# Kernel tuning notes

Measured on AMD Instinct MI355X. Metric: run time of the kernel, lower is better.

The kernel has to match this reference:

```python
import jax, jax.numpy as jnp
import numpy as np

# Model dims (init_kwargs): in_channels=hid_channels=128, freq_bins=64, num_heads=8
B, CIN, HID, FREQ, T, H = 4, 128, 128, 64, 512, 8
EPS = 1e-5  # LayerNormalization4D eps


def _conv_act_norm(y, w, b, alpha, gamma, beta):
    """1x1 Conv2d + PReLU + LayerNormalization4D(C,F) on [B, C_in, T, F].
    w: [C_out, C_in], b: [C_out], alpha: scalar PReLU slope,
    gamma/beta: [1, C_out, 1, F]; normalize over (channel, freq) dims."""
    y = jnp.einsum('bctf,oc->botf', y, w) + b[None, :, None, None]
    y = jnp.where(y >= 0, y, alpha * y)  # PReLU (single shared slope)
    mu = jnp.mean(y, axis=(1, 3), keepdims=True)
    var = jnp.mean(jnp.square(y - mu), axis=(1, 3), keepdims=True)
    return (y - mu) / jnp.sqrt(var + EPS) * gamma + beta


def setup_inputs() -> dict:
    key = jax.random.key(0)
    ks = jax.random.split(key, 6)
    s = 0.02
    return {
        'x': jax.random.normal(ks[0], (B, CIN, FREQ, T), jnp.float32),
        'qkv_w': jax.random.normal(ks[1], (3 * HID, CIN), jnp.float32) * s,
        'qkv_b': jnp.zeros((3 * HID,), jnp.float32),
        'qkv_alpha': jnp.float32(0.25),
        'qkv_gamma': jnp.ones((1, 3 * HID, 1, FREQ), jnp.float32),
        'qkv_beta': jnp.zeros((1, 3 * HID, 1, FREQ), jnp.float32),
        'proj_w': jax.random.normal(ks[2], (CIN, CIN), jnp.float32) * s,
        'proj_b': jnp.zeros((CIN,), jnp.float32),
        'proj_alpha': jnp.float32(0.25),
        'proj_gamma': jnp.ones((1, CIN, 1, FREQ), jnp.float32),
        'proj_beta': jnp.zeros((1, CIN, 1, FREQ), jnp.float32),
    }


def reference(x, qkv_w, qkv_b, qkv_alpha, qkv_gamma, qkv_beta,
              proj_w, proj_b, proj_alpha, proj_gamma, proj_beta):
    # x: [B, C, F, T] -> [B, C, T, F]
    xt = jnp.swapaxes(x, -2, -1)
    qkv = _conv_act_norm(xt, qkv_w, qkv_b, qkv_alpha, qkv_gamma, qkv_beta)  # [B, 3*HID, T, F]
    # [B, T, 3*HID, F] -> heads split over flattened (channel, freq) axis
    qkv = jnp.swapaxes(qkv, 1, 2).reshape(B, T, H, -1)
    qkv = jnp.swapaxes(qkv, 1, 2)  # [B, H, T, 3*hd]
    hd = qkv.shape[-1] // 3
    q = qkv[..., :hd]
    k = qkv[..., hd:2 * hd]
    v = qkv[..., 2 * hd:]
    scores = jnp.einsum('bhqd,bhkd->bhqk', q, k) * (hd ** -0.5)
    causal = jnp.triu(jnp.ones((T, T), bool), 1)
    scores = jnp.where(causal[None, None], -jnp.inf, scores)
    attn = jax.nn.softmax(scores, axis=-1)
    ctx = jnp.einsum('bhqk,bhkd->bhqd', attn, v)  # [B, H, T, hd]
    # mimic torch: reshape(B*H, T, hd).transpose(1,2).reshape(B, HID, T, FREQ)
    c = jnp.swapaxes(ctx.reshape(B * H, T, hd), 1, 2).reshape(B, HID, T, FREQ)
    out = _conv_act_norm(c, proj_w, proj_b, proj_alpha, proj_gamma, proj_beta)
    return jnp.swapaxes(out, 2, 3)  # [B, C, F, T]
```

## Files before the change

kernel.cpp:

```cpp
#include <hip/hip_runtime.h>
#include <hip/hip_bf16.h>

#define T_    512
#define CIN_  128
#define OC1   384
#define NH    8
#define HD    1024

using sh8 = __attribute__((ext_vector_type(8))) short;
using fx4 = __attribute__((ext_vector_type(4))) float;

__device__ __forceinline__ short bf16r(float x) {
  union { float f; unsigned u; } v; v.f = x;
  unsigned u = v.u;
  u += 0x7fffu + ((u >> 16) & 1u);
  return (short)(u >> 16);
}
__device__ __forceinline__ float b2f(short s) {
  union { float f; unsigned u; } v; v.u = ((unsigned)(unsigned short)s) << 16;
  return v.f;
}
__device__ __forceinline__ fx4 mfma_bf16(sh8 a, sh8 b, fx4 c) {
  return __builtin_amdgcn_mfma_f32_16x16x32_bf16(a, b, c, 0, 0, 0);
}

__global__ void k_prep(const float* __restrict__ qw, const float* __restrict__ pw,
                       short* __restrict__ qwb, short* __restrict__ pwb) {
  const int i = blockIdx.x * 256 + threadIdx.x;
  if (i < OC1 * CIN_) qwb[i] = bf16r(qw[i]);
  if (i < 128 * 128)  pwb[i] = bf16r(pw[i]);
}

__global__ __launch_bounds__(512) void kA_qkv(
    const float* __restrict__ x, const short* __restrict__ wb,
    const float* __restrict__ bias, const float* __restrict__ alphap,
    short* __restrict__ Qt, short* __restrict__ Kt, short* __restrict__ Vt,
    float* __restrict__ Pstat)
{
  const int bid = blockIdx.x;
  const int b = bid >> 8, f = (bid >> 2) & 63, tt = bid & 3;
  const int tid = threadIdx.x, lane = tid & 63, w = tid >> 6;

  __shared__ short Xs[128 * 128];
  __shared__ float psum[8 * 8 * 16 * 2];

  {
    const int c = tid & 127, tg = tid >> 7;
    const float* xp = x + ((size_t)(b * 128 + c) * 64 + f) * 512 + tt * 128 + tg * 32;
    #pragma unroll
    for (int i = 0; i < 8; ++i) {
      const float4 fv = *(const float4*)(xp + i * 4);
      #pragma unroll
      for (int j = 0; j < 4; ++j) {
        const int t = tg * 32 + i * 4 + j;
        *((short*)((char*)Xs + t * 256 + ((2 * c) ^ ((t & 7) << 4)))) = bf16r((&fv.x)[j]);
      }
    }
  }
  __syncthreads();

  const float alpha = alphap[0];
  fx4 acc[3][8];
  #pragma unroll
  for (int mi = 0; mi < 3; ++mi)
    #pragma unroll
    for (int ni = 0; ni < 8; ++ni) acc[mi][ni] = fx4{0.f, 0.f, 0.f, 0.f};

  #pragma unroll
  for (int ks = 0; ks < 4; ++ks) {
    sh8 a[3];
    #pragma unroll
    for (int mi = 0; mi < 3; ++mi) {
      const int o = w * 48 + mi * 16 + (lane & 15);
      a[mi] = *(const sh8*)(wb + o * 128 + ks * 32 + (lane >> 4) * 8);
    }
    #pragma unroll
    for (int ni = 0; ni < 8; ++ni) {
      const int t = ni * 16 + (lane & 15);
      const int kb = ks * 64 + (lane >> 4) * 16;
      const sh8 bf = *(const sh8*)((const char*)Xs + t * 256 + (kb ^ ((t & 7) << 4)));
      #pragma unroll
      for (int mi = 0; mi < 3; ++mi)
        acc[mi][ni] = mfma_bf16(a[mi], bf, acc[mi][ni]);
    }
  }

  float s0[8], s1[8];
  #pragma unroll
  for (int ni = 0; ni < 8; ++ni) { s0[ni] = 0.f; s1[ni] = 0.f; }
  #pragma unroll
  for (int mi = 0; mi < 3; ++mi)
    #pragma unroll
    for (int r = 0; r < 4; ++r) {
      const int o = w * 48 + mi * 16 + (lane >> 4) * 4 + r;
      const float bo = bias[o];
      #pragma unroll
      for (int ni = 0; ni < 8; ++ni) {
        float v = acc[mi][ni][r] + bo;
        v = (v >= 0.f) ? v : alpha * v;
        acc[mi][ni][r] = v;
        s0[ni] += v; s1[ni] += v * v;
      }
    }
  #pragma unroll
  for (int ni = 0; ni < 8; ++ni) {
    float a0 = s0[ni], a1 = s1[ni];
    a0 += __shfl_down(a0, 32); a1 += __shfl_down(a1, 32);
    a0 += __shfl_down(a0, 16); a1 += __shfl_down(a1, 16);
    if (lane < 16) {
      psum[((w * 8 + ni) * 16 + lane) * 2 + 0] = a0;
      psum[((w * 8 + ni) * 16 + lane) * 2 + 1] = a1;
    }
  }
  __syncthreads();
  if (tid < 256) {
    const int col = tid & 127, s = tid >> 7;
    const int ni = col >> 4, l = col & 15;
    float a0 = 0.f;
    #pragma unroll
    for (int ww = 0; ww < 8; ++ww) a0 += psum[((ww * 8 + ni) * 16 + l) * 2 + s];
    Pstat[(size_t)s * 131072 + (size_t)b * 32768 + (size_t)f * 512 + tt * 128 + col] = a0;
  }

  const int bh = b * 8 + w;
  #pragma unroll
  for (int mi = 0; mi < 3; ++mi) {
    short* dst = (mi == 0) ? Qt : (mi == 1) ? Kt : Vt;
    #pragma unroll
    for (int r = 0; r < 4; ++r) {
      const int cl = (lane >> 4) * 4 + r;
      const int d = cl * 64 + f;
      short* rowp = dst + ((size_t)bh * 1024 + d) * 512 + tt * 128;
      #pragma unroll
      for (int ni = 0; ni < 8; ++ni)
        rowp[ni * 16 + (lane & 15)] = bf16r(acc[mi][ni][r]);
    }
  }
}

__global__ __launch_bounds__(256) void kB_norm(
    const short* __restrict__ Qt, const short* __restrict__ Kt, short* __restrict__ Vt,
    const float* __restrict__ Pstat,
    const float* __restrict__ gamma, const float* __restrict__ beta,
    short* __restrict__ Q, short* __restrict__ K)
{
  const int bid = blockIdx.x;
  const int bh = bid >> 4, tc = bid & 15;
  const int b = bh >> 3, h = bh & 7;
  const int tid = threadIdx.x, lane = tid & 63, w = tid >> 6;
  const int t0 = tc * 32;

  __shared__ short Lt[32 * 512];
  __shared__ float stats[32][2];

  #pragma unroll
  for (int k = 0; k < 8; ++k) {
    const int tl = w * 8 + k;
    const int t = t0 + tl;
    float p0 = Pstat[(size_t)b * 32768 + (size_t)lane * 512 + t];
    float p1 = Pstat[131072 + (size_t)b * 32768 + (size_t)lane * 512 + t];
    #pragma unroll
    for (int off = 32; off > 0; off >>= 1) { p0 += __shfl_down(p0, off); p1 += __shfl_down(p1, off); }
    if (lane == 0) {
      const float mu = p0 * (1.f / 24576.f);
      const float var = p1 * (1.f / 24576.f) - mu * mu;
      stats[tl][0] = mu;
      stats[tl][1] = rsqrtf(var + 1e-5f);
    }
  }
  __syncthreads();

  for (int sect = 0; sect < 2; ++sect) {
    const short* src = sect ? Kt : Qt;
    short* dstq = sect ? K : Q;
    for (int dh = 0; dh < 2; ++dh) {
      __syncthreads();
      #pragma unroll
      for (int rr = 0; rr < 2; ++rr) {
        const int dl = tid + rr * 256;
        const int d = dh * 512 + dl;
        const int gi = (h * 48 + sect * 16 + (d >> 6)) * 64 + (d & 63);
        const float g = gamma[gi], be = beta[gi];
        const short* srow = src + ((size_t)bh * 1024 + d) * 512 + t0;
        #pragma unroll
        for (int i = 0; i < 4; ++i) {
          const sh8 vv = *(const sh8*)(srow + i * 8);
          #pragma unroll
          for (int j = 0; j < 8; ++j) {
            const int tl = i * 8 + j;
            const float z = (b2f(vv[j]) - stats[tl][0]) * stats[tl][1] * g + be;
            *((short*)((char*)Lt + tl * 1024 + ((2 * dl) ^ ((tl & 7) << 4)))) = bf16r(z);
          }
        }
      }
      __syncthreads();
      const int tl = tid >> 3;
      short* orow = dstq + ((size_t)bh * 512 + (t0 + tl)) * 1024 + dh * 512;
      #pragma unroll
      for (int it = 0; it < 8; ++it) {
        const int c16 = (tid & 7) + it * 8;
        const sh8 vv = *(const sh8*)((const char*)Lt + tl * 1024 + ((c16 * 16) ^ ((tl & 7) << 4)));
        *(sh8*)(orow + c16 * 8) = vv;
      }
    }
  }

  #pragma unroll
  for (int rr = 0; rr < 4; ++rr) {
    const int d = tid + rr * 256;
    const int gi = (h * 48 + 32 + (d >> 6)) * 64 + (d & 63);
    const float g = gamma[gi], be = beta[gi];
    short* vrow = Vt + ((size_t)bh * 1024 + d) * 512 + t0;
    #pragma unroll
    for (int i = 0; i < 4; ++i) {
      sh8 vv = *(const sh8*)(vrow + i * 8);
      #pragma unroll
      for (int j = 0; j < 8; ++j) {
        const int tl = i * 8 + j;
        vv[j] = bf16r((b2f(vv[j]) - stats[tl][0]) * stats[tl][1] * g + be);
      }
      *(sh8*)(vrow + i * 8) = vv;
    }
  }
}

__global__ __launch_bounds__(256) void k_qk(
    const short* __restrict__ Q, const short* __restrict__ K, float* __restrict__ S)
{
  const int bid = blockIdx.x;
  const int bh = bid / 10;
  const int j = bid - bh * 10;
  const int qi = (j >= 6) ? 3 : (j >= 3) ? 2 : (j >= 1) ? 1 : 0;
  const int ki = j - qi * (qi + 1) / 2;
  const int tid = threadIdx.x, lane = tid & 63, w = tid >> 6;
  const int wm = w >> 1, wn = w & 1;

  __shared__ short Qs[128 * 64];
  __shared__ short Ks[128 * 64];

  const short* Qg = Q + ((size_t)bh * 512 + qi * 128) * 1024;
  const short* Kg = K + ((size_t)bh * 512 + ki * 128) * 1024;

  fx4 acc[4][4];
  #pragma unroll
  for (int mi = 0; mi < 4; ++mi)
    #pragma unroll
    for (int ni = 0; ni < 4; ++ni) acc[mi][ni] = fx4{0.f, 0.f, 0.f, 0.f};

  for (int ks = 0; ks < 16; ++ks) {
    __syncthreads();
    const int row = tid & 127, kh = tid >> 7;
    #pragma unroll
    for (int i = 0; i < 4; ++i) {
      const int kl = kh * 32 + i * 8;
      const sh8 qv = *(const sh8*)(Qg + (size_t)row * 1024 + ks * 64 + kl);
      const sh8 kv = *(const sh8*)(Kg + (size_t)row * 1024 + ks * 64 + kl);
      *(sh8*)((char*)Qs + row * 128 + ((2 * kl) ^ ((row & 7) << 4))) = qv;
      *(sh8*)((char*)Ks + row * 128 + ((2 * kl) ^ ((row & 7) << 4))) = kv;
    }
    __syncthreads();
    #pragma unroll
    for (int ksub = 0; ksub < 2; ++ksub) {
      sh8 a[4], bf[4];
      #pragma unroll
      for (int mi = 0; mi < 4; ++mi) {
        const int r2 = wm * 64 + mi * 16 + (lane & 15);
        a[mi] = *(const sh8*)((const char*)Qs + r2 * 128 + ((ksub * 64 + (lane >> 4) * 16) ^ ((r2 & 7) << 4)));
      }
      #pragma unroll
      for (int ni = 0; ni < 4; ++ni) {
        const int r2 = wn * 64 + ni * 16 + (lane & 15);
        bf[ni] = *(const sh8*)((const char*)Ks + r2 * 128 + ((ksub * 64 + (lane >> 4) * 16) ^ ((r2 & 7) << 4)));
      }
      #pragma unroll
      for (int mi = 0; mi < 4; ++mi)
        #pragma unroll
        for (int ni = 0; ni < 4; ++ni)
          acc[mi][ni] = mfma_bf16(a[mi], bf[ni], acc[mi][ni]);
    }
  }

  float* Sg = S + (size_t)bh * 262144;
  const int q0 = qi * 128 + wm * 64, k0 = ki * 128 + wn * 64;
  #pragma unroll
  for (int mi = 0; mi < 4; ++mi)
    #pragma unroll
    for (int ni = 0; ni < 4; ++ni) {
      const int q = q0 + mi * 16 + (lane >> 4) * 4;
      const int kc = k0 + ni * 16 + (lane & 15);
      #pragma unroll
      for (int r = 0; r < 4; ++r)
        Sg[(size_t)(q + r) * 512 + kc] = acc[mi][ni][r] * 0.03125f;
    }
}

__global__ __launch_bounds__(256) void k_softmax(const float* __restrict__ S,
                                                 short* __restrict__ Pb)
{
  const int row = blockIdx.x * 4 + (threadIdx.x >> 6);
  const int lane = threadIdx.x & 63;
  const int bh = row >> 9, q = row & 511;
  const float* Sr = S + (size_t)bh * 262144 + (size_t)q * 512;
  short* Pr = Pb + (size_t)bh * 262144 + (size_t)q * 512;
  const int n = q + 1;
  float v[8]; float mx = -1e30f;
  #pragma unroll
  for (int i = 0; i < 8; ++i) {
    const int k = lane + i * 64;
    v[i] = (k < n) ? Sr[k] : -1e30f;
    mx = fmaxf(mx, v[i]);
  }
  #pragma unroll
  for (int off = 32; off > 0; off >>= 1) mx = fmaxf(mx, __shfl_xor(mx, off));
  float sum = 0.f;
  #pragma unroll
  for (int i = 0; i < 8; ++i) {
    const float e = (v[i] > -1e29f) ? __expf(v[i] - mx) : 0.f;
    v[i] = e; sum += e;
  }
  #pragma unroll
  for (int off = 32; off > 0; off >>= 1) sum += __shfl_xor(sum, off);
  const float inv = 1.f / sum;
  #pragma unroll
  for (int i = 0; i < 8; ++i) Pr[lane + i * 64] = bf16r(v[i] * inv);
}

__global__ __launch_bounds__(256) void k_pv(
    const short* __restrict__ Pb, const short* __restrict__ Vt, short* __restrict__ Cs)
{
  const int bid = blockIdx.x;
  const int bh = bid >> 5;
  const int qi = (bid >> 3) & 3, dt = bid & 7;
  const int tid = threadIdx.x, lane = tid & 63, w = tid >> 6;
  const int wm = w >> 1, wn = w & 1;

  __shared__ short Ps[128 * 64];
  __shared__ short Vs[128 * 64];
  __shared__ short ctile[128 * 128];

  const short* Pg = Pb + ((size_t)bh * 512 + qi * 128) * 512;
  const short* Vg = Vt + ((size_t)bh * 1024 + dt * 128) * 512;

  fx4 acc[4][4];
  #pragma unroll
  for (int mi = 0; mi < 4; ++mi)
    #pragma unroll
    for (int ni = 0; ni < 4; ++ni) acc[mi][ni] = fx4{0.f, 0.f, 0.f, 0.f};

  const int nks = (qi + 1) * 2;
  for (int ks = 0; ks < nks; ++ks) {
    __syncthreads();
    const int row = tid & 127, kh = tid >> 7;
    #pragma unroll
    for (int i = 0; i < 4; ++i) {
      const int kl = kh * 32 + i * 8;
      const sh8 pv = *(const sh8*)(Pg + (size_t)row * 512 + ks * 64 + kl);
      const sh8 vv = *(const sh8*)(Vg + (size_t)row * 512 + ks * 64 + kl);
      *(sh8*)((char*)Ps + row * 128 + ((2 * kl) ^ ((row & 7) << 4))) = pv;
      *(sh8*)((char*)Vs + row * 128 + ((2 * kl) ^ ((row & 7) << 4))) = vv;
    }
    __syncthreads();
    #pragma unroll
    for (int ksub = 0; ksub < 2; ++ksub) {
      sh8 a[4], bf[4];
      #pragma unroll
      for (int mi = 0; mi < 4; ++mi) {
        const int r2 = wm * 64 + mi * 16 + (lane & 15);
        a[mi] = *(const sh8*)((const char*)Ps + r2 * 128 + ((ksub * 64 + (lane >> 4) * 16) ^ ((r2 & 7) << 4)));
      }
      #pragma unroll
      for (int ni = 0; ni < 4; ++ni) {
        const int r2 = wn * 64 + ni * 16 + (lane & 15);
        bf[ni] = *(const sh8*)((const char*)Vs + r2 * 128 + ((ksub * 64 + (lane >> 4) * 16) ^ ((r2 & 7) << 4)));
      }
      #pragma unroll
      for (int mi = 0; mi < 4; ++mi)
        #pragma unroll
        for (int ni = 0; ni < 4; ++ni)
          acc[mi][ni] = mfma_bf16(a[mi], bf[ni], acc[mi][ni]);
    }
  }

  #pragma unroll
  for (int mi = 0; mi < 4; ++mi)
    #pragma unroll
    for (int ni = 0; ni < 4; ++ni) {
      const int ql = wm * 64 + mi * 16 + (lane >> 4) * 4;
      const int dl = wn * 64 + ni * 16 + (lane & 15);
      const int swz = (dl & 7) << 4;
      #pragma unroll
      for (int r = 0; r < 4; ++r)
        ctile[(dl * 256 + ((2 * (ql + r)) ^ swz)) >> 1] = bf16r(acc[mi][ni][r]);
    }
  __syncthreads();

  const int b = bh >> 3, h = bh & 7;
  const int cl_loc = tid >> 7, fq = (tid >> 1) & 63, tg_loc = tid & 1;
  const int C = h * 16 + dt * 2 + cl_loc;
  const int t2 = fq * 8 + qi * 2 + tg_loc;
  const int dl = cl_loc * 64 + fq;
  const int swz = (dl & 7) << 4;
  short* dst = Cs + (((size_t)b * 128 + C) * 512 + t2) * 64;
  #pragma unroll
  for (int jj = 0; jj < 8; ++jj) {
    const sh8 vv = *(const sh8*)((const char*)ctile + dl * 256 + ((tg_loc * 128 + jj * 16) ^ swz));
    *(sh8*)(dst + jj * 8) = vv;
  }
}

__global__ __launch_bounds__(512) void k_proj(
    const short* __restrict__ Cs, const short* __restrict__ wb,
    const float* __restrict__ bias, const float* __restrict__ alphap,
    const float* __restrict__ gamma, const float* __restrict__ beta,
    float* __restrict__ Otmp)
{
  const int bid = blockIdx.x;
  const int b = bid >> 9, t2 = bid & 511;
  const int tid = threadIdx.x, lane = tid & 63, w = tid >> 6;

  __shared__ short Xs[64 * 128];
  __shared__ float red[18];

  {
    const int C = tid & 127, fq = tid >> 7;
    const short* srow = Cs + (((size_t)b * 128 + C) * 512 + t2) * 64;
    #pragma unroll
    for (int i = 0; i < 2; ++i) {
      const int fc = fq * 2 + i;
      const sh8 vv = *(const sh8*)(srow + fc * 8);
      #pragma unroll
      for (int jj = 0; jj < 8; ++jj) {
        const int f2 = fc * 8 + jj;
        *((short*)((char*)Xs + f2 * 256 + ((2 * C) ^ ((f2 & 7) << 4)))) = vv[jj];
      }
    }
  }
  __syncthreads();

  const float alpha = alphap[0];
  fx4 acc[4];
  #pragma unroll
  for (int ni = 0; ni < 4; ++ni) acc[ni] = fx4{0.f, 0.f, 0.f, 0.f};

  #pragma unroll
  for (int ks = 0; ks < 4; ++ks) {
    const int o = w * 16 + (lane & 15);
    const sh8 a = *(const sh8*)(wb + o * 128 + ks * 32 + (lane >> 4) * 8);
    #pragma unroll
    for (int ni = 0; ni < 4; ++ni) {
      const int f2 = ni * 16 + (lane & 15);
      const sh8 bf = *(const sh8*)((const char*)Xs + f2 * 256 + ((ks * 64 + (lane >> 4) * 16) ^ ((f2 & 7) << 4)));
      acc[ni] = mfma_bf16(a, bf, acc[ni]);
    }
  }

  float s0 = 0.f, s1 = 0.f;
  const int ob = w * 16 + (lane >> 4) * 4;
  #pragma unroll
  for (int ni = 0; ni < 4; ++ni)
    #pragma unroll
    for (int r = 0; r < 4; ++r) {
      float v = acc[ni][r] + bias[ob + r];
      v = (v >= 0.f) ? v : alpha * v;
      acc[ni][r] = v;
      s0 += v; s1 += v * v;
    }
  #pragma unroll
  for (int off = 32; off > 0; off >>= 1) { s0 += __shfl_down(s0, off); s1 += __shfl_down(s1, off); }
  if (lane == 0) { red[w * 2] = s0; red[w * 2 + 1] = s1; }
  __syncthreads();
  if (tid == 0) {
    float a0 = 0.f, a1 = 0.f;
    for (int i2 = 0; i2 < 8; ++i2) { a0 += red[2 * i2]; a1 += red[2 * i2 + 1]; }
    const float mu = a0 / 8192.f;
    const float var = a1 / 8192.f - mu * mu;
    red[16] = mu; red[17] = rsqrtf(var + 1e-5f);
  }
  __syncthreads();
  const float mu = red[16], rstd = red[17];

  #pragma unroll
  for (int ni = 0; ni < 4; ++ni) {
    const int f2 = ni * 16 + (lane & 15);
    #pragma unroll
    for (int r = 0; r < 4; ++r) {
      const int o = ob + r;
      const float zz = (acc[ni][r] - mu) * rstd * gamma[o * 64 + f2] + beta[o * 64 + f2];
      Otmp[(((size_t)b * 128 + o) * 512 + t2) * 64 + f2] = zz;
    }
  }
}

__global__ __launch_bounds__(256) void k_trans(const float* __restrict__ Otmp,
                                               float* __restrict__ out)
{
  const int bid = blockIdx.x;
  const int bo = bid >> 3, tt8 = bid & 7;
  const int t20 = tt8 * 64;
  const int tid = threadIdx.x;
  __shared__ float Ltr[64][65];
  {
    const int f2c = tid & 15, t2l0 = tid >> 4;
    #pragma unroll
    for (int it = 0; it < 4; ++it) {
      const int t2l = t2l0 + it * 16;
      const float4 fv = *(const float4*)(Otmp + ((size_t)bo * 512 + t20 + t2l) * 64 + f2c * 4);
      Ltr[f2c * 4 + 0][t2l] = fv.x;
      Ltr[f2c * 4 + 1][t2l] = fv.y;
      Ltr[f2c * 4 + 2][t2l] = fv.z;
      Ltr[f2c * 4 + 3][t2l] = fv.w;
    }
  }
  __syncthreads();
  {
    const int t2c = tid & 15, f2l0 = tid >> 4;
    #pragma unroll
    for (int it = 0; it < 4; ++it) {
      const int f2 = f2l0 + it * 16;
      float4 fv;
      fv.x = Ltr[f2][t2c * 4 + 0]; fv.y = Ltr[f2][t2c * 4 + 1];
      fv.z = Ltr[f2][t2c * 4 + 2]; fv.w = Ltr[f2][t2c * 4 + 3];
      *(float4*)(out + ((size_t)bo * 64 + f2) * 512 + t20 + t2c * 4) = fv;
    }
  }
}

extern "C" void kernel_launch(void* const* d_in, const int* in_sizes, int n_in,
                              void* d_out, int out_size, void* d_ws, size_t ws_size,
                              hipStream_t stream) {
  (void)in_sizes; (void)n_in; (void)out_size;
  const float* x          = (const float*)d_in[0];
  const float* qkv_w      = (const float*)d_in[1];
  const float* qkv_b      = (const float*)d_in[2];
  const float* qkv_alpha  = (const float*)d_in[3];
  const float* qkv_gamma  = (const float*)d_in[4];
  const float* qkv_beta   = (const float*)d_in[5];
  const float* proj_w     = (const float*)d_in[6];
  const float* proj_b     = (const float*)d_in[7];
  const float* proj_alpha = (const float*)d_in[8];
  const float* proj_gamma = (const float*)d_in[9];
  const float* proj_beta  = (const float*)d_in[10];
  float* out = (float*)d_out;

  char* ws = (char*)d_ws;
  short* Qt  = (short*)(ws + 0);
  short* Kt  = (short*)(ws + 33554432);
  short* Vt  = (short*)(ws + 67108864);
  short* Q   = (short*)(ws + 100663296);
  short* K   = (short*)(ws + 134217728);
  short* qwb = (short*)(ws + 167772160);
  short* pwb = (short*)(ws + 167870464);
  float* S    = (float*)(ws + 0);
  short* Pb   = (short*)(ws + 33554432);
  short* Cs   = (short*)(ws + 100663296);
  float* Otmp = (float*)(ws + 0);
  float* Pstat = (float*)d_out;
  if (ws_size < 167903232u) return;

  k_prep<<<192, 256, 0, stream>>>(qkv_w, proj_w, qwb, pwb);
  kA_qkv<<<1024, 512, 0, stream>>>(x, qwb, qkv_b, qkv_alpha, Qt, Kt, Vt, Pstat);
  kB_norm<<<512, 256, 0, stream>>>(Qt, Kt, Vt, Pstat, qkv_gamma, qkv_beta, Q, K);
  k_qk<<<320, 256, 0, stream>>>(Q, K, S);
  k_softmax<<<4096, 256, 0, stream>>>(S, Pb);
  k_pv<<<1024, 256, 0, stream>>>(Pb, Vt, Cs);
  k_proj<<<2048, 512, 0, stream>>>(Cs, pwb, proj_b, proj_alpha, proj_gamma, proj_beta, Otmp);
  k_trans<<<4096, 256, 0, stream>>>(Otmp, out);
}
```

Baseline: 279.0 us.

## Fuse QKV layer-norm into attention GEMM loads and drop the separate norm pass

Removes the standalone normalization kernel. The QKV kernel now writes Q and K unnormalized in a permuted row-major layout, and a tiny stats kernel computes per-time mean and rstd. The QK and PV kernels apply the normalization, with pre-permuted gamma and beta, while staging tiles into shared memory. The projection output intermediate is also stored as bf16 instead of fp32 to halve transpose traffic, at some cost in output precision. This cuts a full read and write pass over the Q, K and V buffers, but adds per-tile normalization arithmetic in the GEMM kernels. The workspace layout is also reshuffled.

```diff
diff --git a/kernel.cpp b/kernel.cpp
--- a/kernel.cpp
+++ b/kernel.cpp
@@ -1,11 +1,7 @@
 #include <hip/hip_runtime.h>
 #include <hip/hip_bf16.h>
 
-#define T_    512
-#define CIN_  128
-#define OC1   384
-#define NH    8
-#define HD    1024
+#define T_ 512
 
 using sh8 = __attribute__((ext_vector_type(8))) short;
 using fx4 = __attribute__((ext_vector_type(4))) float;
@@ -24,17 +20,33 @@
   return __builtin_amdgcn_mfma_f32_16x16x32_bf16(a, b, c, 0, 0, 0);
 }
 
-__global__ void k_prep(const float* __restrict__ qw, const float* __restrict__ pw,
-                       short* __restrict__ qwb, short* __restrict__ pwb) {
+__global__ __launch_bounds__(256) void k_prep(
+    const float* __restrict__ qw, const float* __restrict__ pw,
+    const float* __restrict__ gamma, const float* __restrict__ beta,
+    short* __restrict__ qwb, short* __restrict__ pwb,
+    float* __restrict__ gq, float* __restrict__ bq,
+    float* __restrict__ gv, float* __restrict__ bv)
+{
   const int i = blockIdx.x * 256 + threadIdx.x;
-  if (i < OC1 * CIN_) qwb[i] = bf16r(qw[i]);
-  if (i < 128 * 128)  pwb[i] = bf16r(pw[i]);
+  if (i < 49152) qwb[i] = bf16r(qw[i]);
+  if (i < 16384) pwb[i] = bf16r(pw[i]);
+  if (i < 16384) {
+    const int sh = i >> 10, dp = i & 1023;
+    const int sect = sh >> 3, h = sh & 7;
+    const int gi = (h * 48 + sect * 16 + (dp & 15)) * 64 + (dp >> 4);
+    gq[i] = gamma[gi]; bq[i] = beta[gi];
+  }
+  if (i < 8192) {
+    const int h = i >> 10, d = i & 1023;
+    const int gi = (h * 48 + 32 + (d >> 6)) * 64 + (d & 63);
+    gv[i] = gamma[gi]; bv[i] = beta[gi];
+  }
 }
 
 __global__ __launch_bounds__(512) void kA_qkv(
     const float* __restrict__ x, const short* __restrict__ wb,
     const float* __restrict__ bias, const float* __restrict__ alphap,
-    short* __restrict__ Qt, short* __restrict__ Kt, short* __restrict__ Vt,
+    short* __restrict__ Qp, short* __restrict__ Kp, short* __restrict__ Vt,
     float* __restrict__ Pstat)
 {
   const int bid = blockIdx.x;
@@ -42,18 +54,21 @@
   const int tid = threadIdx.x, lane = tid & 63, w = tid >> 6;
 
   __shared__ short Xs[128 * 128];
-  __shared__ float psum[8 * 8 * 16 * 2];
+  __shared__ float psum[2048];
 
   {
-    const int c = tid & 127, tg = tid >> 7;
-    const float* xp = x + ((size_t)(b * 128 + c) * 64 + f) * 512 + tt * 128 + tg * 32;
-    #pragma unroll
-    for (int i = 0; i < 8; ++i) {
-      const float4 fv = *(const float4*)(xp + i * 4);
-      #pragma unroll
-      for (int j = 0; j < 4; ++j) {
-        const int t = tg * 32 + i * 4 + j;
-        *((short*)((char*)Xs + t * 256 + ((2 * c) ^ ((t & 7) << 4)))) = bf16r((&fv.x)[j]);
+    const int c0 = tid >> 5, tl = (tid & 31) * 2;
+    const float* xb = x + ((size_t)(b * 128) * 64 + f) * 512 + tt * 128;
+    #pragma unroll
+    for (int p = 0; p < 8; ++p) {
+      const int c = c0 + p * 16;
+      const float* xp = xb + (size_t)c * 32768;
+      #pragma unroll
+      for (int q = 0; q < 2; ++q) {
+        const int t = q * 64 + tl;
+        const float2 fv = *(const float2*)(xp + t);
+        *((short*)((char*)Xs + (t    ) * 256 + ((2 * c) ^ (((t    ) & 7) << 4)))) = bf16r(fv.x);
+        *((short*)((char*)Xs + (t + 1) * 256 + ((2 * c) ^ (((t + 1) & 7) << 4)))) = bf16r(fv.y);
       }
     }
   }
@@ -77,8 +92,8 @@
     #pragma unroll
     for (int ni = 0; ni < 8; ++ni) {
       const int t = ni * 16 + (lane & 15);
-      const int kb = ks * 64 + (lane >> 4) * 16;
-      const sh8 bf = *(const sh8*)((const char*)Xs + t * 256 + (kb ^ ((t & 7) << 4)));
+      const sh8 bf = *(const sh8*)((const char*)Xs + t * 256 +
+                     ((ks * 64 + (lane >> 4) * 16) ^ ((t & 7) << 4)));
       #pragma unroll
       for (int mi = 0; mi < 3; ++mi)
         acc[mi][ni] = mfma_bf16(a[mi], bf, acc[mi][ni]);
@@ -124,122 +139,77 @@
 
   const int bh = b * 8 + w;
   #pragma unroll
-  for (int mi = 0; mi < 3; ++mi) {
-    short* dst = (mi == 0) ? Qt : (mi == 1) ? Kt : Vt;
+  for (int mi = 0; mi < 2; ++mi) {
+    short* dst = mi ? Kp : Qp;
+    #pragma unroll
+    for (int ni = 0; ni < 8; ++ni) {
+      const int t = tt * 128 + ni * 16 + (lane & 15);
+      const unsigned lo = (unsigned)(unsigned short)bf16r(acc[mi][ni][0]) |
+                          ((unsigned)(unsigned short)bf16r(acc[mi][ni][1]) << 16);
+      const unsigned hi = (unsigned)(unsigned short)bf16r(acc[mi][ni][2]) |
+                          ((unsigned)(unsigned short)bf16r(acc[mi][ni][3]) << 16);
+      uint2 pk; pk.x = lo; pk.y = hi;
+      *(uint2*)(dst + ((size_t)bh * 512 + t) * 1024 + f * 16 + (lane >> 4) * 4) = pk;
+    }
+  }
+  #pragma unroll
+  for (int ni = 0; ni < 8; ++ni)
     #pragma unroll
     for (int r = 0; r < 4; ++r) {
       const int cl = (lane >> 4) * 4 + r;
-      const int d = cl * 64 + f;
-      short* rowp = dst + ((size_t)bh * 1024 + d) * 512 + tt * 128;
-      #pragma unroll
-      for (int ni = 0; ni < 8; ++ni)
-        rowp[ni * 16 + (lane & 15)] = bf16r(acc[mi][ni][r]);
-    }
-  }
-}
-
-__global__ __launch_bounds__(256) void kB_norm(
-    const short* __restrict__ Qt, const short* __restrict__ Kt, short* __restrict__ Vt,
-    const float* __restrict__ Pstat,
-    const float* __restrict__ gamma, const float* __restrict__ beta,
-    short* __restrict__ Q, short* __restrict__ K)
-{
-  const int bid = blockIdx.x;
-  const int bh = bid >> 4, tc = bid & 15;
-  const int b = bh >> 3, h = bh & 7;
-  const int tid = threadIdx.x, lane = tid & 63, w = tid >> 6;
-  const int t0 = tc * 32;
-
-  __shared__ short Lt[32 * 512];
-  __shared__ float stats[32][2];
-
-  #pragma unroll
-  for (int k = 0; k < 8; ++k) {
-    const int tl = w * 8 + k;
-    const int t = t0 + tl;
-    float p0 = Pstat[(size_t)b * 32768 + (size_t)lane * 512 + t];
-    float p1 = Pstat[131072 + (size_t)b * 32768 + (size_t)lane * 512 + t];
-    #pragma unroll
-    for (int off = 32; off > 0; off >>= 1) { p0 += __shfl_down(p0, off); p1 += __shfl_down(p1, off); }
-    if (lane == 0) {
-      const float mu = p0 * (1.f / 24576.f);
-      const float var = p1 * (1.f / 24576.f) - mu * mu;
-      stats[tl][0] = mu;
-      stats[tl][1] = rsqrtf(var + 1e-5f);
-    }
-  }
-  __syncthreads();
-
-  for (int sect = 0; sect < 2; ++sect) {
-    const short* src = sect ? Kt : Qt;
-    short* dstq = sect ? K : Q;
-    for (int dh = 0; dh < 2; ++dh) {
-      __syncthreads();
-      #pragma unroll
-      for (int rr = 0; rr < 2; ++rr) {
-        const int dl = tid + rr * 256;
-        const int d = dh * 512 + dl;
-        const int gi = (h * 48 + sect * 16 + (d >> 6)) * 64 + (d & 63);
-        const float g = gamma[gi], be = beta[gi];
-        const short* srow = src + ((size_t)bh * 1024 + d) * 512 + t0;
-        #pragma unroll
-        for (int i = 0; i < 4; ++i) {
-          const sh8 vv = *(const sh8*)(srow + i * 8);
-          #pragma unroll
-          for (int j = 0; j < 8; ++j) {
-            const int tl = i * 8 + j;
-            const float z = (b2f(vv[j]) - stats[tl][0]) * stats[tl][1] * g + be;
-            *((short*)((char*)Lt + tl * 1024 + ((2 * dl) ^ ((tl & 7) << 4)))) = bf16r(z);
-          }
-        }
-      }
-      __syncthreads();
-      const int tl = tid >> 3;
-      short* orow = dstq + ((size_t)bh * 512 + (t0 + tl)) * 1024 + dh * 512;
-      #pragma unroll
-      for (int it = 0; it < 8; ++it) {
-        const int c16 = (tid & 7) + it * 8;
-        const sh8 vv = *(const sh8*)((const char*)Lt + tl * 1024 + ((c16 * 16) ^ ((tl & 7) << 4)));
-        *(sh8*)(orow + c16 * 8) = vv;
-      }
-    }
-  }
-
-  #pragma unroll
-  for (int rr = 0; rr < 4; ++rr) {
-    const int d = tid + rr * 256;
-    const int gi = (h * 48 + 32 + (d >> 6)) * 64 + (d & 63);
-    const float g = gamma[gi], be = beta[gi];
-    short* vrow = Vt + ((size_t)bh * 1024 + d) * 512 + t0;
-    #pragma unroll
-    for (int i = 0; i < 4; ++i) {
-      sh8 vv = *(const sh8*)(vrow + i * 8);
-      #pragma unroll
-      for (int j = 0; j < 8; ++j) {
-        const int tl = i * 8 + j;
-        vv[j] = bf16r((b2f(vv[j]) - stats[tl][0]) * stats[tl][1] * g + be);
-      }
-      *(sh8*)(vrow + i * 8) = vv;
-    }
-  }
+      Vt[((size_t)bh * 1024 + cl * 64 + f) * 512 + tt * 128 + ni * 16 + (lane & 15)] =
+          bf16r(acc[2][ni][r]);
+    }
+}
+
+__global__ __launch_bounds__(256) void k_stats(const float* __restrict__ Pstat,
+                                               float* __restrict__ MuRs)
+{
+  const int idx = blockIdx.x * 256 + threadIdx.x;
+  const int b = idx >> 9, t = idx & 511;
+  float s0 = 0.f, s1 = 0.f;
+  for (int f = 0; f < 64; ++f) {
+    s0 += Pstat[((size_t)b * 64 + f) * 512 + t];
+    s1 += Pstat[131072 + ((size_t)b * 64 + f) * 512 + t];
+  }
+  const float mu = s0 * (1.f / 24576.f);
+  const float var = s1 * (1.f / 24576.f) - mu * mu;
+  MuRs[idx * 2] = mu;
+  MuRs[idx * 2 + 1] = rsqrtf(var + 1e-5f);
 }
 
 __global__ __launch_bounds__(256) void k_qk(
-    const short* __restrict__ Q, const short* __restrict__ K, float* __restrict__ S)
+    const short* __restrict__ Qp, const short* __restrict__ Kp,
+    const float* __restrict__ MuRs, const float* __restrict__ gq,
+    const float* __restrict__ bq, float* __restrict__ S)
 {
   const int bid = blockIdx.x;
   const int bh = bid / 10;
   const int j = bid - bh * 10;
   const int qi = (j >= 6) ? 3 : (j >= 3) ? 2 : (j >= 1) ? 1 : 0;
   const int ki = j - qi * (qi + 1) / 2;
+  const int b = bh >> 3, h = bh & 7;
   const int tid = threadIdx.x, lane = tid & 63, w = tid >> 6;
   const int wm = w >> 1, wn = w & 1;
 
-  __shared__ short Qs[128 * 64];
-  __shared__ short Ks[128 * 64];
-
-  const short* Qg = Q + ((size_t)bh * 512 + qi * 128) * 1024;
-  const short* Kg = K + ((size_t)bh * 512 + ki * 128) * 1024;
+  __shared__ short Qs[128 * 128];
+  __shared__ short Ks[128 * 128];
+  __shared__ float sQ[256], sK[256];
+
+  if (tid < 128) {
+    *(float2*)&sQ[tid * 2] = *(const float2*)(MuRs + ((size_t)b * 512 + qi * 128 + tid) * 2);
+    *(float2*)&sK[tid * 2] = *(const float2*)(MuRs + ((size_t)b * 512 + ki * 128 + tid) * 2);
+  }
+  __syncthreads();
+
+  const int op = tid >> 7;
+  const int rowslot = (tid >> 4) & 7, unit = tid & 15;
+  const short* src = op ? (Kp + ((size_t)bh * 512 + ki * 128) * 1024)
+                        : (Qp + ((size_t)bh * 512 + qi * 128) * 1024);
+  const float* murs = op ? sK : sQ;
+  short* dstl = op ? Ks : Qs;
+  const float* gqp = gq + (size_t)(op * 8 + h) * 1024;
+  const float* bqp = bq + (size_t)(op * 8 + h) * 1024;
 
   fx4 acc[4][4];
   #pragma unroll
@@ -247,36 +217,45 @@
     #pragma unroll
     for (int ni = 0; ni < 4; ++ni) acc[mi][ni] = fx4{0.f, 0.f, 0.f, 0.f};
 
-  for (int ks = 0; ks < 16; ++ks) {
+  for (int ks = 0; ks < 8; ++ks) {
+    float g8[8], b8[8];
+    *(float4*)&g8[0] = *(const float4*)(gqp + ks * 128 + unit * 8);
+    *(float4*)&g8[4] = *(const float4*)(gqp + ks * 128 + unit * 8 + 4);
+    *(float4*)&b8[0] = *(const float4*)(bqp + ks * 128 + unit * 8);
+    *(float4*)&b8[4] = *(const float4*)(bqp + ks * 128 + unit * 8 + 4);
     __syncthreads();
-    const int row = tid & 127, kh = tid >> 7;
-    #pragma unroll
-    for (int i = 0; i < 4; ++i) {
-      const int kl = kh * 32 + i * 8;
-      const sh8 qv = *(const sh8*)(Qg + (size_t)row * 1024 + ks * 64 + kl);
-      const sh8 kv = *(const sh8*)(Kg + (size_t)row * 1024 + ks * 64 + kl);
-      *(sh8*)((char*)Qs + row * 128 + ((2 * kl) ^ ((row & 7) << 4))) = qv;
-      *(sh8*)((char*)Ks + row * 128 + ((2 * kl) ^ ((row & 7) << 4))) = kv;
+    #pragma unroll
+    for (int rit = 0; rit < 16; ++rit) {
+      const int row = rit * 8 + rowslot;
+      const sh8 v = *(const sh8*)(src + (size_t)row * 1024 + ks * 128 + unit * 8);
+      const float mu = murs[row * 2], rs = murs[row * 2 + 1];
+      sh8 o;
+      #pragma unroll
+      for (int e = 0; e < 8; ++e)
+        o[e] = bf16r((b2f(v[e]) - mu) * rs * g8[e] + b8[e]);
+      *(sh8*)((char*)dstl + row * 256 + ((unit * 16) ^ ((row & 7) << 4))) = o;
     }
     __syncthreads();
     #pragma unroll
-    for (int ksub = 0; ksub < 2; ++ksub) {
-      sh8 a[4], bf[4];
+    for (int ksub = 0; ksub < 4; ++ksub) {
+      sh8 a[4], bb[4];
       #pragma unroll
       for (int mi = 0; mi < 4; ++mi) {
-        const int r2 = wm * 64 + mi * 16 + (lane & 15);
-        a[mi] = *(const sh8*)((const char*)Qs + r2 * 128 + ((ksub * 64 + (lane >> 4) * 16) ^ ((r2 & 7) << 4)));
+        const int t = wm * 64 + mi * 16 + (lane & 15);
+        a[mi] = *(const sh8*)((const char*)Qs + t * 256 +
+                ((ksub * 64 + (lane >> 4) * 16) ^ ((t & 7) << 4)));
       }
       #pragma unroll
       for (int ni = 0; ni < 4; ++ni) {
-        const int r2 = wn * 64 + ni * 16 + (lane & 15);
-        bf[ni] = *(const sh8*)((const char*)Ks + r2 * 128 + ((ksub * 64 + (lane >> 4) * 16) ^ ((r2 & 7) << 4)));
+        const int t = wn * 64 + ni * 16 + (lane & 15);
+        bb[ni] = *(const sh8*)((const char*)Ks + t * 256 +
+                 ((ksub * 64 + (lane >> 4) * 16) ^ ((t & 7) << 4)));
       }
       #pragma unroll
       for (int mi = 0; mi < 4; ++mi)
         #pragma unroll
         for (int ni = 0; ni < 4; ++ni)
-          acc[mi][ni] = mfma_bf16(a[mi], bf[ni], acc[mi][ni]);
+          acc[mi][ni] = mfma_bf16(a[mi], bb[ni], acc[mi][ni]);
     }
   }
 
@@ -326,20 +305,28 @@
 }
 
 __global__ __launch_bounds__(256) void k_pv(
-    const short* __restrict__ Pb, const short* __restrict__ Vt, short* __restrict__ Cs)
+    const short* __restrict__ Pb, const short* __restrict__ Vt,
+    const float* __restrict__ MuRs, const float* __restrict__ gv,
+    const float* __restrict__ bv, short* __restrict__ Cs)
 {
   const int bid = blockIdx.x;
-  const int bh = bid >> 5;
-  const int qi = (bid >> 3) & 3, dt = bid & 7;
+  const int bh = bid >> 5, qi = (bid >> 3) & 3, dt = bid & 7;
+  const int b = bh >> 3, h = bh & 7;
   const int tid = threadIdx.x, lane = tid & 63, w = tid >> 6;
   const int wm = w >> 1, wn = w & 1;
 
-  __shared__ short Ps[128 * 64];
-  __shared__ short Vs[128 * 64];
-  __shared__ short ctile[128 * 128];
+  __shared__ char smem[32768];
+  short* Ps = (short*)smem;
+  short* Vs = (short*)(smem + 16384);
+  short* ctile = (short*)smem;
 
   const short* Pg = Pb + ((size_t)bh * 512 + qi * 128) * 512;
   const short* Vg = Vt + ((size_t)bh * 1024 + dt * 128) * 512;
+  const float* gvp = gv + (size_t)h * 1024 + dt * 128;
+  const float* bvp = bv + (size_t)h * 1024 + dt * 128;
+  const float* mrp = MuRs + (size_t)b * 1024;
+
+  const int rowslot = tid >> 3, unit = tid & 7;
 
   fx4 acc[4][4];
   #pragma unroll
@@ -349,37 +336,49 @@
 
   const int nks = (qi + 1) * 2;
   for (int ks = 0; ks < nks; ++ks) {
+    float mr[16];
+    *(float4*)&mr[0]  = *(const float4*)(mrp + (ks * 64 + unit * 8) * 2);
+    *(float4*)&mr[4]  = *(const float4*)(mrp + (ks * 64 + unit * 8) * 2 + 4);
+    *(float4*)&mr[8]  = *(const float4*)(mrp + (ks * 64 + unit * 8) * 2 + 8);
+    *(float4*)&mr[12] = *(const float4*)(mrp + (ks * 64 + unit * 8) * 2 + 12);
     __syncthreads();
-    const int row = tid & 127, kh = tid >> 7;
-    #pragma unroll
-    for (int i = 0; i < 4; ++i) {
-      const int kl = kh * 32 + i * 8;
-      const sh8 pv = *(const sh8*)(Pg + (size_t)row * 512 + ks * 64 + kl);
-      const sh8 vv = *(const sh8*)(Vg + (size_t)row * 512 + ks * 64 + kl);
-      *(sh8*)((char*)Ps + row * 128 + ((2 * kl) ^ ((row & 7) << 4))) = pv;
-      *(sh8*)((char*)Vs + row * 128 + ((2 * kl) ^ ((row & 7) << 4))) = vv;
+    #pragma unroll
+    for (int rit = 0; rit < 4; ++rit) {
+      const int row = rit * 32 + rowslot;
+      const sh8 p = *(const sh8*)(Pg + (size_t)row * 512 + ks * 64 + unit * 8);
+      *(sh8*)((char*)Ps + row * 128 + ((unit * 16) ^ ((row & 7) << 4))) = p;
+      const sh8 vv = *(const sh8*)(Vg + (size_t)row * 512 + ks * 64 + unit * 8);
+      const float g = gvp[row], be = bvp[row];
+      sh8 o;
+      #pragma unroll
+      for (int e = 0; e < 8; ++e)
+        o[e] = bf16r((b2f(vv[e]) - mr[e * 2]) * mr[e * 2 + 1] * g + be);
+      *(sh8*)((char*)Vs + row * 128 + ((unit * 16) ^ ((row & 7) << 4))) = o;
     }
     __syncthreads();
     #pragma unroll
     for (int ksub = 0; ksub < 2; ++ksub) {
-      sh8 a[4], bf[4];
+      sh8 a[4], bb[4];
       #pragma unroll
       for (int mi = 0; mi < 4; ++mi) {
         const int r2 = wm * 64 + mi * 16 + (lane & 15);
-        a[mi] = *(const sh8*)((const char*)Ps + r2 * 128 + ((ksub * 64 + (lane >> 4) * 16) ^ ((r2 & 7) << 4)));
+        a[mi] = *(const sh8*)((const char*)Ps + r2 * 128 +
+                ((ksub * 64 + (lane >> 4) * 16) ^ ((r2 & 7) << 4)));
       }
       #pragma unroll
       for (int ni = 0; ni < 4; ++ni) {
         const int r2 = wn * 64 + ni * 16 + (lane & 15);
-        bf[ni] = *(const sh8*)((const char*)Vs + r2 * 128 + ((ksub * 64 + (lane >> 4) * 16) ^ ((r2 & 7) << 4)));
+        bb[ni] = *(const sh8*)((const char*)Vs + r2 * 128 +
+                 ((ksub * 64 + (lane >> 4) * 16) ^ ((r2 & 7) << 4)));
       }
       #pragma unroll
       for (int mi = 0; mi < 4; ++mi)
         #pragma unroll
         for (int ni = 0; ni < 4; ++ni)
-          acc[mi][ni] = mfma_bf16(a[mi], bf[ni], acc[mi][ni]);
-    }
-  }
+          acc[mi][ni] = mfma_bf16(a[mi], bb[ni], acc[mi][ni]);
+    }
+  }
+  __syncthreads();
 
   #pragma unroll
   for (int mi = 0; mi < 4; ++mi)
@@ -394,7 +393,6 @@
     }
   __syncthreads();
 
-  const int b = bh >> 3, h = bh & 7;
   const int cl_loc = tid >> 7, fq = (tid >> 1) & 63, tg_loc = tid & 1;
   const int C = h * 16 + dt * 2 + cl_loc;
   const int t2 = fq * 8 + qi * 2 + tg_loc;
@@ -412,7 +410,7 @@
     const short* __restrict__ Cs, const short* __restrict__ wb,
     const float* __restrict__ bias, const float* __restrict__ alphap,
     const float* __restrict__ gamma, const float* __restrict__ beta,
-    float* __restrict__ Otmp)
+    short* __restrict__ Otmpb)
 {
   const int bid = blockIdx.x;
   const int b = bid >> 9, t2 = bid & 511;
@@ -422,15 +420,14 @@
   __shared__ float red[18];
 
   {
-    const int C = tid & 127, fq = tid >> 7;
-    const short* srow = Cs + (((size_t)b * 128 + C) * 512 + t2) * 64;
-    #pragma unroll
-    for (int i = 0; i < 2; ++i) {
-      const int fc = fq * 2 + i;
-      const sh8 vv = *(const sh8*)(srow + fc * 8);
+    const int rowslot = tid >> 3, unit = tid & 7;
+    #pragma unroll
+    for (int rit = 0; rit < 2; ++rit) {
+      const int C = rit * 64 + rowslot;
+      const sh8 vv = *(const sh8*)(Cs + (((size_t)b * 128 + C) * 512 + t2) * 64 + unit * 8);
       #pragma unroll
       for (int jj = 0; jj < 8; ++jj) {
-        const int f2 = fc * 8 + jj;
+        const int f2 = unit * 8 + jj;
         *((short*)((char*)Xs + f2 * 256 + ((2 * C) ^ ((f2 & 7) << 4)))) = vv[jj];
       }
     }
@@ -449,7 +446,8 @@
     #pragma unroll
     for (int ni = 0; ni < 4; ++ni) {
       const int f2 = ni * 16 + (lane & 15);
-      const sh8 bf = *(const sh8*)((const char*)Xs + f2 * 256 + ((ks * 64 + (lane >> 4) * 16) ^ ((f2 & 7) << 4)));
+      const sh8 bf = *(const sh8*)((const char*)Xs + f2 * 256 +
+                     ((ks * 64 + (lane >> 4) * 16) ^ ((f2 & 7) << 4)));
       acc[ni] = mfma_bf16(a, bf, acc[ni]);
     }
   }
@@ -486,42 +484,38 @@
     for (int r = 0; r < 4; ++r) {
       const int o = ob + r;
       const float zz = (acc[ni][r] - mu) * rstd * gamma[o * 64 + f2] + beta[o * 64 + f2];
-      Otmp[(((size_t)b * 128 + o) * 512 + t2) * 64 + f2] = zz;
-    }
-  }
-}
-
-__global__ __launch_bounds__(256) void k_trans(const float* __restrict__ Otmp,
+      Otmpb[(((size_t)b * 128 + o) * 512 + t2) * 64 + f2] = bf16r(zz);
+    }
+  }
+}
+
+__global__ __launch_bounds__(256) void k_trans(const short* __restrict__ Otmpb,
                                                float* __restrict__ out)
 {
   const int bid = blockIdx.x;
   const int bo = bid >> 3, tt8 = bid & 7;
   const int t20 = tt8 * 64;
   const int tid = threadIdx.x;
-  __shared__ float Ltr[64][65];
+  __shared__ float Ltr[64 * 68];
+
   {
-    const int f2c = tid & 15, t2l0 = tid >> 4;
-    #pragma unroll
-    for (int it = 0; it < 4; ++it) {
-      const int t2l = t2l0 + it * 16;
-      const float4 fv = *(const float4*)(Otmp + ((size_t)bo * 512 + t20 + t2l) * 64 + f2c * 4);
-      Ltr[f2c * 4 + 0][t2l] = fv.x;
-      Ltr[f2c * 4 + 1][t2l] = fv.y;
-      Ltr[f2c * 4 + 2][t2l] = fv.z;
-      Ltr[f2c * 4 + 3][t2l] = fv.w;
+    const int t2l = tid >> 2, u = tid & 3;
+    const short* srow = Otmpb + ((size_t)bo * 512 + t20 + t2l) * 64 + u * 16;
+    const sh8 v0 = *(const sh8*)(srow);
+    const sh8 v1 = *(const sh8*)(srow + 8);
+    #pragma unroll
+    for (int e = 0; e < 8; ++e) {
+      Ltr[(u * 16 + e) * 68 + t2l]     = b2f(v0[e]);
+      Ltr[(u * 16 + 8 + e) * 68 + t2l] = b2f(v1[e]);
     }
   }
   __syncthreads();
   {
-    const int t2c = tid & 15, f2l0 = tid >> 4;
-    #pragma unroll
-    for (int it = 0; it < 4; ++it) {
-      const int f2 = f2l0 + it * 16;
-      float4 fv;
-      fv.x = Ltr[f2][t2c * 4 + 0]; fv.y = Ltr[f2][t2c * 4 + 1];
-      fv.z = Ltr[f2][t2c * 4 + 2]; fv.w = Ltr[f2][t2c * 4 + 3];
-      *(float4*)(out + ((size_t)bo * 64 + f2) * 512 + t20 + t2c * 4) = fv;
-    }
+    const int f2 = tid >> 2, u = tid & 3;
+    float* dst = out + ((size_t)bo * 64 + f2) * 512 + t20 + u * 16;
+    #pragma unroll
+    for (int k = 0; k < 4; ++k)
+      *(float4*)(dst + k * 4) = *(const float4*)&Ltr[f2 * 68 + u * 16 + k * 4];
   }
 }
 
@@ -543,26 +537,30 @@
   float* out = (float*)d_out;
 
   char* ws = (char*)d_ws;
-  short* Qt  = (short*)(ws + 0);
-  short* Kt  = (short*)(ws + 33554432);
-  short* Vt  = (short*)(ws + 67108864);
-  short* Q   = (short*)(ws + 100663296);
-  short* K   = (short*)(ws + 134217728);
-  short* qwb = (short*)(ws + 167772160);
-  short* pwb = (short*)(ws + 167870464);
-  float* S    = (float*)(ws + 0);
-  short* Pb   = (short*)(ws + 33554432);
-  short* Cs   = (short*)(ws + 100663296);
-  float* Otmp = (float*)(ws + 0);
+  short* Qp   = (short*)(ws + 0);
+  short* Kp   = (short*)(ws + 33554432);
+  short* Vt   = (short*)(ws + 67108864);
+  float* S    = (float*)(ws + 100663296);
+  short* Pb   = (short*)(ws + 134217728);
+  float* MuRs = (float*)(ws + 150994944);
+  float* gq   = (float*)(ws + 151011328);
+  float* bq   = (float*)(ws + 151076864);
+  float* gv   = (float*)(ws + 151142400);
+  float* bv   = (float*)(ws + 151175168);
+  short* Cs    = (short*)(ws + 0);
+  short* Otmpb = (short*)(ws + 33554432);
+  short* qwb  = (short*)(ws + 167772160);
+  short* pwb  = (short*)(ws + 167870464);
   float* Pstat = (float*)d_out;
   if (ws_size < 167903232u) return;
 
-  k_prep<<<192, 256, 0, stream>>>(qkv_w, proj_w, qwb, pwb);
-  kA_qkv<<<1024, 512, 0, stream>>>(x, qwb, qkv_b, qkv_alpha, Qt, Kt, Vt, Pstat);
-  kB_norm<<<512, 256, 0, stream>>>(Qt, Kt, Vt, Pstat, qkv_gamma, qkv_beta, Q, K);
-  k_qk<<<320, 256, 0, stream>>>(Q, K, S);
+  k_prep<<<192, 256, 0, stream>>>(qkv_w, proj_w, qkv_gamma, qkv_beta,
+                                  qwb, pwb, gq, bq, gv, bv);
+  kA_qkv<<<1024, 512, 0, stream>>>(x, qwb, qkv_b, qkv_alpha, Qp, Kp, Vt, Pstat);
+  k_stats<<<8, 256, 0, stream>>>(Pstat, MuRs);
+  k_qk<<<320, 256, 0, stream>>>(Qp, Kp, MuRs, gq, bq, S);
   k_softmax<<<4096, 256, 0, stream>>>(S, Pb);
-  k_pv<<<1024, 256, 0, stream>>>(Pb, Vt, Cs);
-  k_proj<<<2048, 512, 0, stream>>>(Cs, pwb, proj_b, proj_alpha, proj_gamma, proj_beta, Otmp);
-  k_trans<<<4096, 256, 0, stream>>>(Otmp, out);
-}
+  k_pv<<<1024, 256, 0, stream>>>(Pb, Vt, MuRs, gv, bv, Cs);
+  k_proj<<<2048, 512, 0, stream>>>(Cs, pwb, proj_b, proj_alpha, proj_gamma, proj_beta, Otmpb);
+  k_trans<<<4096, 256, 0, stream>>>(Otmpb, out);
+}
```

Result: faster. 241.3 us (-13.5%).
